# Kernel optimization log

Measured on AMD Instinct MI355X. Metric: run time of the kernel, lower is better.

## Reference

```python
import jax, jax.numpy as jnp
import numpy as np

B, N, DEG = 64, 512, 16        # graphs, nodes per graph, avg degree
C, HID = 10, 128               # input feat dim (== num_classes quirk), hidden
E = B * N * DEG                # total edges (fixed; pooling masks edges)


def _gcn(x, W, b, src, dst, emask, n):
    # PyG GCNConv: add self-loops, symmetric norm D^-1/2 (A+I) D^-1/2 (XW) + b
    h = x @ W
    deg = jax.ops.segment_sum(emask, dst, num_segments=n) + 1.0  # +1 self-loop
    dinv = jax.lax.rsqrt(deg)
    norm = dinv[src] * dinv[dst] * emask
    agg = jax.ops.segment_sum(h[src] * norm[:, None], dst, num_segments=n)
    return agg + h * (dinv * dinv)[:, None] + b  # self-loop term + bias


def _sag_pool(x, src, dst, emask, Wp, bp, n_per):
    # SAGPooling: score = tanh(GCN(x)); per-graph top-k (ratio=0.5); x' = x[perm]*score
    n = x.shape[0]
    score = jnp.tanh(_gcn(x, Wp, bp, src, dst, emask, n)[:, 0])
    k = n_per // 2
    vals, idx = jax.lax.top_k(score.reshape(B, n_per), k)  # [B,k]
    perm = (idx + (jnp.arange(B) * n_per)[:, None]).reshape(-1)
    xk = x[perm] * vals.reshape(-1)[:, None]
    # relabel edges; drop edges touching removed nodes via mask (fixed E)
    mapping = jnp.full((n,), -1, jnp.int32).at[perm].set(
        jnp.arange(B * k, dtype=jnp.int32))
    ns, nd = mapping[src], mapping[dst]
    nmask = emask * ((ns >= 0) & (nd >= 0)).astype(emask.dtype)
    return xk, jnp.maximum(ns, 0), jnp.maximum(nd, 0), nmask, k


def _readout(x, k):
    # global max pool || global mean pool (all kept nodes are real, no padding)
    xg = x.reshape(B, k, -1)
    return jnp.concatenate([xg.max(axis=1), xg.mean(axis=1)], axis=1)


def setup_inputs() -> dict:
    key = jax.random.key(0)
    ks = jax.random.split(key, 16)
    x = jax.random.normal(ks[0], (B * N, C), jnp.float32)
    off = jnp.repeat(jnp.arange(B, dtype=jnp.int32) * N, N * DEG)
    src = jax.random.randint(ks[1], (E,), 0, N, jnp.int32) + off
    dst = jax.random.randint(ks[2], (E,), 0, N, jnp.int32) + off
    p = lambda k, s: jax.random.normal(k, s, jnp.float32) * 0.05
    return {
        "x": x, "src": src, "dst": dst,
        "W1": p(ks[3], (C, HID)), "b1": jnp.zeros((HID,), jnp.float32),
        "W2": p(ks[4], (HID, HID)), "b2": jnp.zeros((HID,), jnp.float32),
        "W3": p(ks[5], (HID, HID)), "b3": jnp.zeros((HID,), jnp.float32),
        "Wp": p(ks[6], (HID, 1)), "bp": jnp.zeros((1,), jnp.float32),
        "L1W": p(ks[7], (2 * HID, HID)), "L1b": jnp.zeros((HID,), jnp.float32),
        "L2W": p(ks[8], (HID, HID // 2)), "L2b": jnp.zeros((HID // 2,), jnp.float32),
    }


def reference(x, src, dst, W1, b1, W2, b2, W3, b3, Wp, bp, L1W, L1b, L2W, L2b):
    emask = jnp.ones((E,), jnp.float32)
    h = jax.nn.relu(_gcn(x, W1, b1, src, dst, emask, B * N))
    h, src, dst, emask, k = _sag_pool(h, src, dst, emask, Wp, bp, N)
    x1 = _readout(h, k)
    h = jax.nn.relu(_gcn(h, W2, b2, src, dst, emask, B * k))
    h, src, dst, emask, k = _sag_pool(h, src, dst, emask, Wp, bp, k)
    x2 = _readout(h, k)
    h = jax.nn.relu(_gcn(h, W3, b3, src, dst, emask, B * k))
    h, src, dst, emask, k = _sag_pool(h, src, dst, emask, Wp, bp, k)
    x3 = _readout(h, k)
    z = x1 + x2 + x3
    z = jax.nn.relu(z @ L1W + L1b)
    # dropout inactive in eval mode
    z = jax.nn.relu(z @ L2W + L2b)
    return jax.nn.log_softmax(z, axis=1)
```

## Files before the change

### kernel.cpp

```cpp
#include <hip/hip_runtime.h>
#include <math.h>

#define BGR 64
#define N0 512
#define E_TOT (BGR*N0*16)
#define EPG 8192
#define EIT 16
#define HID 128


__device__ __forceinline__ int2 ldcoh(const int2* p){
  unsigned long long v = __hip_atomic_load(
      (const unsigned long long*)p, __ATOMIC_RELAXED, __HIP_MEMORY_SCOPE_AGENT);
  int2 r; r.x = (int)(unsigned int)v; r.y = (int)(unsigned int)(v >> 32);
  return r;
}

template<bool COH>
__device__ __forceinline__ int2 lde(const int2* p){
  if (COH) return ldcoh(p);
  return *p;
}

template<bool COH>
__device__ __forceinline__ float score_edges(const int2* __restrict__ csr,
    int start, int c, const float* hloc, int gbase){
  float a = 0.f; int j = 0;
  for (; j + 4 <= c; j += 4){
    int2 e0 = lde<COH>(csr+start+j),   e1 = lde<COH>(csr+start+j+1);
    int2 e2 = lde<COH>(csr+start+j+2), e3 = lde<COH>(csr+start+j+3);
    a += __int_as_float(e0.y)*hloc[e0.x - gbase]
       + __int_as_float(e1.y)*hloc[e1.x - gbase]
       + __int_as_float(e2.y)*hloc[e2.x - gbase]
       + __int_as_float(e3.y)*hloc[e3.x - gbase];
  }
  for (; j < c; j++){
    int2 e = lde<COH>(csr+start+j);
    a += __int_as_float(e.y)*hloc[e.x - gbase];
  }
  return a;
}

__device__ __forceinline__ float4 row_edges_coh(const int2* __restrict__ csr,
    int start, int c, const float4* h4, int gbase, int l){
  float4 acc = make_float4(0.f,0.f,0.f,0.f);
  int j = 0;
  for (; j + 4 <= c; j += 4){
    int2 e0 = ldcoh(csr+start+j),   e1 = ldcoh(csr+start+j+1);
    int2 e2 = ldcoh(csr+start+j+2), e3 = ldcoh(csr+start+j+3);
    float4 h0 = h4[(e0.x - gbase)*32 + l];
    float4 h1 = h4[(e1.x - gbase)*32 + l];
    float4 h2 = h4[(e2.x - gbase)*32 + l];
    float4 h3 = h4[(e3.x - gbase)*32 + l];
    float w0 = __int_as_float(e0.y), w1 = __int_as_float(e1.y);
    float w2 = __int_as_float(e2.y), w3 = __int_as_float(e3.y);
    acc.x += w0*h0.x + w1*h1.x + w2*h2.x + w3*h3.x;
    acc.y += w0*h0.y + w1*h1.y + w2*h2.y + w3*h3.y;
    acc.z += w0*h0.z + w1*h1.z + w2*h2.z + w3*h3.z;
    acc.w += w0*h0.w + w1*h1.w + w2*h2.w + w3*h3.w;
  }
  for (; j < c; j++){
    int2 e = ldcoh(csr+start+j);
    float wgt = __int_as_float(e.y);
    float4 hv = h4[(e.x - gbase)*32 + l];
    acc.x += wgt*hv.x; acc.y += wgt*hv.y; acc.z += wgt*hv.z; acc.w += wgt*hv.w;
  }
  return acc;
}

__device__ __forceinline__ void bitonic_sort(float* sv, int* si, float v, int idx,
                                             int t, int nper, bool act){
  for (int kk = 2; kk <= nper; kk <<= 1){
    for (int jj = kk >> 1; jj > 0; jj >>= 1){
      if (jj >= 64){
        if (act){ sv[t] = v; si[t] = idx; }
        __syncthreads();
        if (act){
          int p = t ^ jj;
          float pv = sv[p]; int pi = si[p];
          bool amLower = (t & jj) == 0;
          bool dirDesc = (t & kk) == 0;
          bool betterMine = (v > pv) || (v == pv && idx < pi);
          if ((amLower == dirDesc) != betterMine){ v = pv; idx = pi; }
        }
        __syncthreads();
      } else if (act){
        float pv = __shfl_xor(v, jj);
        int   pi = __shfl_xor(idx, jj);
        bool amLower = (t & jj) == 0;
        bool dirDesc = (t & kk) == 0;
        bool betterMine = (v > pv) || (v == pv && idx < pi);
        if ((amLower == dirDesc) != betterMine){ v = pv; idx = pi; }
      }
    }
  }
  if (act){ sv[t] = v; si[t] = idx; }
  __syncthreads();
}

template<bool COH>
__device__ __forceinline__ void relabel(int2* __restrict__ edges,
    int2* __restrict__ csr, const int* si, int* map, int* sb, int* cur,
    float* dl, int* rpl, int* cntl, int t, int nper, int k,
    int gbase, int ebase){
  if (t < nper) map[t] = -1;
  if (t < k) sb[t] = 0;
  __syncthreads();
  if (t < k) map[si[t]] = t;
  __syncthreads();
  int2 ebuf[EIT];
  #pragma unroll
  for (int it = 0; it < EIT; it++){
    int i = ebase + it*512 + t;
    int2 e = lde<COH>(edges + i);
    int2 ne = make_int2(-1, 0);
    if (e.x >= 0){
      int ns = map[e.x - gbase], nd = map[e.y - gbase];
      if (ns >= 0 && nd >= 0){
        ne = make_int2(gbase + ns, gbase + nd);
        atomicAdd(&sb[nd], 1);
      }
    }
    ebuf[it] = ne;
    edges[i] = ne;
  }
  __syncthreads();
  int vdeg = (t < k) ? sb[t] : 0;
  for (int off = 1; off < k; off <<= 1){
    int add = (t >= off && t < k) ? sb[t-off] : 0;
    __syncthreads();
    if (t < k) sb[t] += add;
    __syncthreads();
  }
  if (t < k){
    int excl = sb[t] - vdeg;
    rpl[t] = ebase + excl;
    cntl[t] = vdeg;
    cur[t] = excl;
    float dv = rsqrtf((float)vdeg + 1.f);
    dl[t] = dv;
  }
  __syncthreads();
  #pragma unroll
  for (int it = 0; it < EIT; it++){
    int2 e = ebuf[it];
    if (e.x >= 0){
      int sl = e.x - gbase, dc = e.y - gbase;
      int pos = atomicAdd(&cur[dc], 1);
      csr[ebase + pos] = make_int2(e.x, __float_as_int(dl[sl]*dl[dc]));
    }
  }
  __syncthreads();
}

__device__ __forceinline__ void gemm_inplace(float* xl, const float* __restrict__ W,
                                             int nn, int t){
  float4* xl4 = (float4*)xl;
  int fq = t & 31;
  int ng = t >> 5;
  for (int tb = 0; tb < nn; tb += 64){
    int n0 = tb + ng*4;
    float4 acc[4];
    #pragma unroll
    for (int c = 0; c < 4; c++) acc[c] = make_float4(0.f,0.f,0.f,0.f);
    for (int i = 0; i < HID; i += 4){
      float4 w0 = *(const float4*)(W + (i+0)*HID + fq*4);
      float4 w1 = *(const float4*)(W + (i+1)*HID + fq*4);
      float4 w2 = *(const float4*)(W + (i+2)*HID + fq*4);
      float4 w3 = *(const float4*)(W + (i+3)*HID + fq*4);
      #pragma unroll
      for (int c = 0; c < 4; c++){
        float4 xv = *(const float4*)(xl + (n0+c)*HID + i);
        acc[c].x += xv.x*w0.x; acc[c].x += xv.y*w1.x;
        acc[c].x += xv.z*w2.x; acc[c].x += xv.w*w3.x;
        acc[c].y += xv.x*w0.y; acc[c].y += xv.y*w1.y;
        acc[c].y += xv.z*w2.y; acc[c].y += xv.w*w3.y;
        acc[c].z += xv.x*w0.z; acc[c].z += xv.y*w1.z;
        acc[c].z += xv.z*w2.z; acc[c].z += xv.w*w3.z;
        acc[c].w += xv.x*w0.w; acc[c].w += xv.y*w1.w;
        acc[c].w += xv.z*w2.w; acc[c].w += xv.w*w3.w;
      }
    }
    __syncthreads();
    #pragma unroll
    for (int c = 0; c < 4; c++)
      xl4[(n0+c)*32 + fq] = acc[c];
  }
  __syncthreads();
}

__global__ __launch_bounds__(512) void k_topo0(
    const int* __restrict__ s0, const int* __restrict__ d0,
    int2* __restrict__ edges, int* __restrict__ cnt, int* __restrict__ rowptr,
    float* __restrict__ dinv, int2* __restrict__ csr){
  __shared__ int   deg[512];
  __shared__ int   sb[512];
  __shared__ int   cur[512];
  __shared__ float dl[512];
  int g = (blockIdx.x & 7)*8 + (blockIdx.x >> 3);
  int t = threadIdx.x;
  int gbase = g*N0, ebase = g*EPG;
  deg[t] = 0;
  __syncthreads();
  int2 ebuf[EIT];
  #pragma unroll
  for (int it = 0; it < EIT; it++){
    int i = ebase + it*512 + t;
    int2 e = make_int2(s0[i], d0[i]);
    ebuf[it] = e;
    edges[i] = e;
    atomicAdd(&deg[e.y - gbase], 1);
  }
  __syncthreads();
  int vdeg = deg[t];
  sb[t] = vdeg; __syncthreads();
  for (int off = 1; off < 512; off <<= 1){
    int add = (t >= off) ? sb[t-off] : 0;
    __syncthreads(); sb[t] += add; __syncthreads();
  }
  int excl = sb[t] - vdeg;
  rowptr[gbase + t] = ebase + excl;
  cnt[gbase + t] = vdeg;
  cur[t] = excl;
  float dv = rsqrtf((float)vdeg + 1.f);
  dl[t] = dv;
  dinv[gbase + t] = dv;
  __syncthreads();
  #pragma unroll
  for (int it = 0; it < EIT; it++){
    int2 e = ebuf[it];
    int sl = e.x - gbase, dc = e.y - gbase;
    int pos = atomicAdd(&cur[dc], 1);
    csr[ebase + pos] = make_int2(e.x, __float_as_int(dl[sl]*dl[dc]));
  }
}

__global__ __launch_bounds__(512) void k_l1_fused(
    const float* __restrict__ x, const float* __restrict__ W1,
    const int2* __restrict__ csr, const int* __restrict__ rowptr,
    const int* __restrict__ cnt, const float* __restrict__ dinv,
    const float* __restrict__ b1, const float* __restrict__ Wp,
    float4* __restrict__ gout4, float* __restrict__ hp_part){
  extern __shared__ float hl[];
  int b = blockIdx.x;
  int xcd = b & 7, idx = b >> 3;
  int graph = xcd*8 + (idx >> 3);
  int sub = idx & 7;
  int qf = sub >> 1, half = sub & 1;
  int t = threadIdx.x;
  int gbase = graph*N0;
  int fp = t & 31;
  int f = qf*32 + fp;
  float wcol[10];
  #pragma unroll
  for (int k = 0; k < 10; k++) wcol[k] = W1[k*HID + f];
  for (int n = t >> 5; n < N0; n += 16){
    const float* xr = x + (gbase + n)*10;
    float acc = 0.f;
    #pragma unroll
    for (int k = 0; k < 10; k++) acc += xr[k]*wcol[k];
    hl[n*32 + fp] = acc;
  }
  __syncthreads();
  const float4* hl4 = (const float4*)hl;
  int l = t & 7, grp = t >> 3;
  float4 bb = ((const float4*)b1)[qf*8 + l];
  float4 wp = ((const float4*)Wp)[qf*8 + l];
  int n0 = half*256;
  for (int nl = n0 + grp; nl < n0 + 256; nl += 64){
    int node = gbase + nl;
    int start = rowptr[node], c = cnt[node];
    float4 acc = make_float4(0.f,0.f,0.f,0.f);
    int j = 0;
    for (; j + 4 <= c; j += 4){
      int2 e0 = csr[start+j],   e1 = csr[start+j+1];
      int2 e2 = csr[start+j+2], e3 = csr[start+j+3];
      float4 h0 = hl4[(e0.x - gbase)*8 + l];
      float4 h1 = hl4[(e1.x - gbase)*8 + l];
      float4 h2 = hl4[(e2.x - gbase)*8 + l];
      float4 h3 = hl4[(e3.x - gbase)*8 + l];
      float w0 = __int_as_float(e0.y), w1 = __int_as_float(e1.y);
      float w2 = __int_as_float(e2.y), w3 = __int_as_float(e3.y);
      acc.x += w0*h0.x + w1*h1.x + w2*h2.x + w3*h3.x;
      acc.y += w0*h0.y + w1*h1.y + w2*h2.y + w3*h3.y;
      acc.z += w0*h0.z + w1*h1.z + w2*h2.z + w3*h3.z;
      acc.w += w0*h0.w + w1*h1.w + w2*h2.w + w3*h3.w;
    }
    for (; j < c; j++){
      int2 e = csr[start + j];
      float wgt = __int_as_float(e.y);
      float4 hv = hl4[(e.x - gbase)*8 + l];
      acc.x += wgt*hv.x; acc.y += wgt*hv.y; acc.z += wgt*hv.z; acc.w += wgt*hv.w;
    }
    float di = dinv[node], dd = di*di;
    float4 hs = hl4[nl*8 + l];
    float4 v;
    v.x = fmaxf(acc.x + hs.x*dd + bb.x, 0.f);
    v.y = fmaxf(acc.y + hs.y*dd + bb.y, 0.f);
    v.z = fmaxf(acc.z + hs.z*dd + bb.z, 0.f);
    v.w = fmaxf(acc.w + hs.w*dd + bb.w, 0.f);
    gout4[node*32 + qf*8 + l] = v;
    float contrib = v.x*wp.x + v.y*wp.y + v.z*wp.z + v.w*wp.w;
    #pragma unroll
    for (int off = 4; off; off >>= 1) contrib += __shfl_down(contrib, off, 8);
    if (l == 0) hp_part[qf*32768 + node] = contrib;
  }
}

__global__ __launch_bounds__(512) void k_tail(
    const float4* __restrict__ gout4, const float* __restrict__ hp_part,
    int2* __restrict__ csr, int2* __restrict__ edges,
    const int* __restrict__ rowptr1, const int* __restrict__ cnt1,
    const float* __restrict__ dinv1, const float* __restrict__ bp,
    const float* __restrict__ W2, const float* __restrict__ b2,
    const float* __restrict__ W3, const float* __restrict__ b3,
    const float* __restrict__ Wp,
    const float* __restrict__ L1W, const float* __restrict__ L1b,
    const float* __restrict__ L2W, const float* __restrict__ L2b,
    float* __restrict__ out){
  __shared__ float xl[256*HID];
  __shared__ float sv[512];
  __shared__ int   si[512];
  __shared__ float hpl[512];
  __shared__ union UU {
    struct { int map[512]; int sb[512]; int cur[256]; } r;
    float4 pr[2][16][32];
  } u;
  __shared__ float dl[256];
  __shared__ int   rpl[256];
  __shared__ int   cntl[256];
  __shared__ float zacc[256];
  __shared__ float red[2];

  int g = (blockIdx.x & 7)*8 + (blockIdx.x >> 3);
  int t = threadIdx.x;
  int gbase = g*N0, ebase = g*EPG;
  int l = t & 31, j0 = t >> 5;
  float4* xl4 = (float4*)xl;
  float bp0 = bp[0];

  {
    int node = gbase + t;
    hpl[t] = hp_part[node] + hp_part[32768 + node]
           + hp_part[65536 + node] + hp_part[98304 + node];
  }
  __syncthreads();
  {
    int start = rowptr1[gbase + t], c = cnt1[gbase + t];
    float a = score_edges<false>(csr, start, c, hpl, gbase);
    float di = dinv1[gbase + t];
    float v = tanhf(a + hpl[t]*di*di + bp0);
    bitonic_sort(sv, si, v, t, t, 512, true);
  }
  {
    float4 mx = make_float4(-INFINITY,-INFINITY,-INFINITY,-INFINITY);
    float4 sm = make_float4(0.f,0.f,0.f,0.f);
    for (int j = j0; j < 256; j += 16){
      float val = sv[j]; int row = si[j];
      float4 hv = gout4[(gbase + row)*32 + l];
      float4 o = make_float4(hv.x*val, hv.y*val, hv.z*val, hv.w*val);
      xl4[j*32 + l] = o;
      mx.x = fmaxf(mx.x, o.x); mx.y = fmaxf(mx.y, o.y);
      mx.z = fmaxf(mx.z, o.z); mx.w = fmaxf(mx.w, o.w);
      sm.x += o.x; sm.y += o.y; sm.z += o.z; sm.w += o.w;
    }
    u.pr[0][j0][l] = mx; u.pr[1][j0][l] = sm;
    __syncthreads();
    if (t < 32){
      float4 M = u.pr[0][0][t], S = u.pr[1][0][t];
      #pragma unroll
      for (int q = 1; q < 16; q++){
        float4 m2 = u.pr[0][q][t], s2 = u.pr[1][q][t];
        M.x = fmaxf(M.x, m2.x); M.y = fmaxf(M.y, m2.y);
        M.z = fmaxf(M.z, m2.z); M.w = fmaxf(M.w, m2.w);
        S.x += s2.x; S.y += s2.y; S.z += s2.z; S.w += s2.w;
      }
      float ki = 1.f/256.f;
      zacc[t*4+0] = M.x; zacc[t*4+1] = M.y; zacc[t*4+2] = M.z; zacc[t*4+3] = M.w;
      zacc[128+t*4+0] = S.x*ki; zacc[128+t*4+1] = S.y*ki;
      zacc[128+t*4+2] = S.z*ki; zacc[128+t*4+3] = S.w*ki;
    }
    __syncthreads();
  }
  relabel<false>(edges, csr, si, u.r.map, u.r.sb, u.r.cur, dl, rpl, cntl,
                 t, 512, 256, gbase, ebase);

  gemm_inplace(xl, W2, 256, t);
  {
    float4 bb = ((const float4*)b2)[l];
    float4 wp = ((const float4*)Wp)[l];
    for (int r = 0; r < 16; r++){
      int n = r*16 + j0;
      float4 acc = row_edges_coh(csr, rpl[n], cntl[n], xl4, gbase, l);
      float di = dl[n], dd = di*di;
      float4 hs = xl4[n*32 + l];
      float4 v;
      v.x = fmaxf(acc.x + hs.x*dd + bb.x, 0.f);
      v.y = fmaxf(acc.y + hs.y*dd + bb.y, 0.f);
      v.z = fmaxf(acc.z + hs.z*dd + bb.z, 0.f);
      v.w = fmaxf(acc.w + hs.w*dd + bb.w, 0.f);
      float contrib = v.x*wp.x + v.y*wp.y + v.z*wp.z + v.w*wp.w;
      #pragma unroll
      for (int off = 16; off; off >>= 1) contrib += __shfl_down(contrib, off, 32);
      if (l == 0) hpl[n] = contrib;
    }
  }
  __syncthreads();

  {
    float v = 0.f;
    if (t < 256){
      float a = score_edges<true>(csr, rpl[t], cntl[t], hpl, gbase);
      float di = dl[t];
      v = tanhf(a + hpl[t]*di*di + bp0);
    }
    bitonic_sort(sv, si, v, t, t, 256, t < 256);
  }
  {
    float4 bb = ((const float4*)b2)[l];
    float4 o[8];
    float4 mx = make_float4(-INFINITY,-INFINITY,-INFINITY,-INFINITY);
    float4 sm = make_float4(0.f,0.f,0.f,0.f);
    #pragma unroll
    for (int r = 0; r < 8; r++){
      int j = j0 + 16*r;
      float val = sv[j]; int row = si[j];
      float4 acc = row_edges_coh(csr, rpl[row], cntl[row], xl4, gbase, l);
      float di = dl[row], dd = di*di;
      float4 hs = xl4[row*32 + l];
      float4 v;
      v.x = fmaxf(acc.x + hs.x*dd + bb.x, 0.f);
      v.y = fmaxf(acc.y + hs.y*dd + bb.y, 0.f);
      v.z = fmaxf(acc.z + hs.z*dd + bb.z, 0.f);
      v.w = fmaxf(acc.w + hs.w*dd + bb.w, 0.f);
      float4 ov = make_float4(v.x*val, v.y*val, v.z*val, v.w*val);
      o[r] = ov;
      mx.x = fmaxf(mx.x, ov.x); mx.y = fmaxf(mx.y, ov.y);
      mx.z = fmaxf(mx.z, ov.z); mx.w = fmaxf(mx.w, ov.w);
      sm.x += ov.x; sm.y += ov.y; sm.z += ov.z; sm.w += ov.w;
    }
    u.pr[0][j0][l] = mx; u.pr[1][j0][l] = sm;
    __syncthreads();
    #pragma unroll
    for (int r = 0; r < 8; r++){ int j = j0 + 16*r; xl4[j*32 + l] = o[r]; }
    if (t < 32){
      float4 M = u.pr[0][0][t], S = u.pr[1][0][t];
      #pragma unroll
      for (int q = 1; q < 16; q++){
        float4 m2 = u.pr[0][q][t], s2 = u.pr[1][q][t];
        M.x = fmaxf(M.x, m2.x); M.y = fmaxf(M.y, m2.y);
        M.z = fmaxf(M.z, m2.z); M.w = fmaxf(M.w, m2.w);
        S.x += s2.x; S.y += s2.y; S.z += s2.z; S.w += s2.w;
      }
      float ki = 1.f/128.f;
      zacc[t*4+0] += M.x; zacc[t*4+1] += M.y; zacc[t*4+2] += M.z; zacc[t*4+3] += M.w;
      zacc[128+t*4+0] += S.x*ki; zacc[128+t*4+1] += S.y*ki;
      zacc[128+t*4+2] += S.z*ki; zacc[128+t*4+3] += S.w*ki;
    }
    __syncthreads();
  }
  relabel<true>(edges, csr, si, u.r.map, u.r.sb, u.r.cur, dl, rpl, cntl,
                t, 256, 128, gbase, ebase);

  gemm_inplace(xl, W3, 128, t);
  {
    float4 bb = ((const float4*)b3)[l];
    float4 wp = ((const float4*)Wp)[l];
    for (int r = 0; r < 8; r++){
      int n = r*16 + j0;
      float4 acc = row_edges_coh(csr, rpl[n], cntl[n], xl4, gbase, l);
      float di = dl[n], dd = di*di;
      float4 hs = xl4[n*32 + l];
      float4 v;
      v.x = fmaxf(acc.x + hs.x*dd + bb.x, 0.f);
      v.y = fmaxf(acc.y + hs.y*dd + bb.y, 0.f);
      v.z = fmaxf(acc.z + hs.z*dd + bb.z, 0.f);
      v.w = fmaxf(acc.w + hs.w*dd + bb.w, 0.f);
      float contrib = v.x*wp.x + v.y*wp.y + v.z*wp.z + v.w*wp.w;
      #pragma unroll
      for (int off = 16; off; off >>= 1) contrib += __shfl_down(contrib, off, 32);
      if (l == 0) hpl[n] = contrib;
    }
  }
  __syncthreads();

  {
    float v = 0.f;
    if (t < 128){
      float a = score_edges<true>(csr, rpl[t], cntl[t], hpl, gbase);
      float di = dl[t];
      v = tanhf(a + hpl[t]*di*di + bp0);
    }
    bitonic_sort(sv, si, v, t, t, 128, t < 128);
  }
  {
    float4 bb = ((const float4*)b3)[l];
    float4 mx = make_float4(-INFINITY,-INFINITY,-INFINITY,-INFINITY);
    float4 sm = make_float4(0.f,0.f,0.f,0.f);
    #pragma unroll
    for (int r = 0; r < 4; r++){
      int j = j0 + 16*r;
      float val = sv[j]; int row = si[j];
      float4 acc = row_edges_coh(csr, rpl[row], cntl[row], xl4, gbase, l);
      float di = dl[row], dd = di*di;
      float4 hs = xl4[row*32 + l];
      float4 v;
      v.x = fmaxf(acc.x + hs.x*dd + bb.x, 0.f);
      v.y = fmaxf(acc.y + hs.y*dd + bb.y, 0.f);
      v.z = fmaxf(acc.z + hs.z*dd + bb.z, 0.f);
      v.w = fmaxf(acc.w + hs.w*dd + bb.w, 0.f);
      float4 ov = make_float4(v.x*val, v.y*val, v.z*val, v.w*val);
      mx.x = fmaxf(mx.x, ov.x); mx.y = fmaxf(mx.y, ov.y);
      mx.z = fmaxf(mx.z, ov.z); mx.w = fmaxf(mx.w, ov.w);
      sm.x += ov.x; sm.y += ov.y; sm.z += ov.z; sm.w += ov.w;
    }
    u.pr[0][j0][l] = mx; u.pr[1][j0][l] = sm;
    __syncthreads();
    if (t < 32){
      float4 M = u.pr[0][0][t], S = u.pr[1][0][t];
      #pragma unroll
      for (int q = 1; q < 16; q++){
        float4 m2 = u.pr[0][q][t], s2 = u.pr[1][q][t];
        M.x = fmaxf(M.x, m2.x); M.y = fmaxf(M.y, m2.y);
        M.z = fmaxf(M.z, m2.z); M.w = fmaxf(M.w, m2.w);
        S.x += s2.x; S.y += s2.y; S.z += s2.z; S.w += s2.w;
      }
      float ki = 1.f/64.f;
      zacc[t*4+0] += M.x; zacc[t*4+1] += M.y; zacc[t*4+2] += M.z; zacc[t*4+3] += M.w;
      zacc[128+t*4+0] += S.x*ki; zacc[128+t*4+1] += S.y*ki;
      zacc[128+t*4+2] += S.z*ki; zacc[128+t*4+3] += S.w*ki;
    }
    __syncthreads();
  }
  if (t < 128){
    float a = L1b[t];
    for (int i = 0; i < 256; i++) a += zacc[i]*L1W[i*128 + t];
    sv[t] = fmaxf(a, 0.f);
  }
  __syncthreads();
  if (t < 64){
    float a = L2b[t];
    for (int i = 0; i < 128; i++) a += sv[i]*L2W[i*64 + t];
    hpl[t] = fmaxf(a, 0.f);
  }
  __syncthreads();
  if (t == 0){
    float mxv = -INFINITY;
    for (int i = 0; i < 64; i++) mxv = fmaxf(mxv, hpl[i]);
    float s = 0.f;
    for (int i = 0; i < 64; i++) s += expf(hpl[i] - mxv);
    red[0] = mxv; red[1] = logf(s);
  }
  __syncthreads();
  if (t < 64) out[g*64 + t] = hpl[t] - red[0] - red[1];
}

extern "C" void kernel_launch(void* const* d_in, const int* in_sizes, int n_in,
                              void* d_out, int out_size, void* d_ws, size_t ws_size,
                              hipStream_t stream){
  (void)in_sizes; (void)n_in; (void)out_size; (void)ws_size;
  const float* x0  = (const float*)d_in[0];
  const int*   s0  = (const int*)  d_in[1];
  const int*   d0  = (const int*)  d_in[2];
  const float* W1  = (const float*)d_in[3];  const float* b1 = (const float*)d_in[4];
  const float* W2  = (const float*)d_in[5];  const float* b2 = (const float*)d_in[6];
  const float* W3  = (const float*)d_in[7];  const float* b3 = (const float*)d_in[8];
  const float* Wp  = (const float*)d_in[9];  const float* bp = (const float*)d_in[10];
  const float* L1W = (const float*)d_in[11]; const float* L1b = (const float*)d_in[12];
  const float* L2W = (const float*)d_in[13]; const float* L2b = (const float*)d_in[14];
  float* out = (float*)d_out;

  float* w = (float*)d_ws;
  float* gout  = w; w += 32768*HID;
  float* dinvv = w; w += 32768;
  float* hppt  = w; w += 4*32768;
  int* cnt     = (int*)w; w += 32768;
  int* rowptr  = (int*)w; w += 32768;
  int2* edges  = (int2*)w; w += 2*E_TOT;
  int2* csr    = (int2*)w; w += 2*E_TOT;

  k_topo0<<<BGR, 512, 0, stream>>>(s0, d0, edges, cnt, rowptr, dinvv, csr);
  k_l1_fused<<<512, 512, 65536, stream>>>(x0, W1, csr, rowptr, cnt, dinvv,
                                          b1, Wp, (float4*)gout, hppt);
  k_tail<<<BGR, 512, 0, stream>>>((const float4*)gout, hppt, csr, edges,
                                  rowptr, cnt, dinvv, bp, W2, b2, W3, b3, Wp,
                                  L1W, L1b, L2W, L2b, out);
}
```

Before: 268.0 us.

## Split tail kernel across four blocks per graph with feature-slice partitioning

The tail kernel previously ran one block per graph (64 blocks). It now launches four blocks per graph, each owning a 32-wide feature slice, and uses spin-wait global barriers on per-graph atomic counters to exchange partial pooling scores and activations through global memory. Each block redundantly recomputes the top-k selection and edge relabeling on its own copy of the edge and CSR buffers. Shared memory per block shrinks and uses an XOR-swizzled layout to avoid bank conflicts. This adds global traffic, a redundant topology pass per block, and a risk of deadlock if the four blocks of a graph are not co-resident.

```diff
diff --git a/kernel.cpp b/kernel.cpp
--- a/kernel.cpp
+++ b/kernel.cpp
@@ -7,6 +7,8 @@
 #define EPG 8192
 #define EIT 16
 #define HID 128
+
+#define XLI(row,l4) (((row)<<3) | (((l4) ^ (row)) & 7))
 
 
 __device__ __forceinline__ int2 ldcoh(const int2* p){
@@ -41,17 +43,18 @@
   return a;
 }
 
-__device__ __forceinline__ float4 row_edges_coh(const int2* __restrict__ csr,
-    int start, int c, const float4* h4, int gbase, int l){
+__device__ __forceinline__ float4 gcn_row(const int2* __restrict__ csr,
+    int start, int c, const float4* xl4, int gbase, int l, int row,
+    float dd, float4 bb){
   float4 acc = make_float4(0.f,0.f,0.f,0.f);
   int j = 0;
   for (; j + 4 <= c; j += 4){
-    int2 e0 = ldcoh(csr+start+j),   e1 = ldcoh(csr+start+j+1);
-    int2 e2 = ldcoh(csr+start+j+2), e3 = ldcoh(csr+start+j+3);
-    float4 h0 = h4[(e0.x - gbase)*32 + l];
-    float4 h1 = h4[(e1.x - gbase)*32 + l];
-    float4 h2 = h4[(e2.x - gbase)*32 + l];
-    float4 h3 = h4[(e3.x - gbase)*32 + l];
+    int2 e0 = csr[start+j],   e1 = csr[start+j+1];
+    int2 e2 = csr[start+j+2], e3 = csr[start+j+3];
+    float4 h0 = xl4[XLI(e0.x - gbase, l)];
+    float4 h1 = xl4[XLI(e1.x - gbase, l)];
+    float4 h2 = xl4[XLI(e2.x - gbase, l)];
+    float4 h3 = xl4[XLI(e3.x - gbase, l)];
     float w0 = __int_as_float(e0.y), w1 = __int_as_float(e1.y);
     float w2 = __int_as_float(e2.y), w3 = __int_as_float(e3.y);
     acc.x += w0*h0.x + w1*h1.x + w2*h2.x + w3*h3.x;
@@ -60,12 +63,18 @@
     acc.w += w0*h0.w + w1*h1.w + w2*h2.w + w3*h3.w;
   }
   for (; j < c; j++){
-    int2 e = ldcoh(csr+start+j);
+    int2 e = csr[start + j];
     float wgt = __int_as_float(e.y);
-    float4 hv = h4[(e.x - gbase)*32 + l];
+    float4 hv = xl4[XLI(e.x - gbase, l)];
     acc.x += wgt*hv.x; acc.y += wgt*hv.y; acc.z += wgt*hv.z; acc.w += wgt*hv.w;
   }
-  return acc;
+  float4 hs = xl4[XLI(row, l)];
+  float4 v;
+  v.x = fmaxf(acc.x + hs.x*dd + bb.x, 0.f);
+  v.y = fmaxf(acc.y + hs.y*dd + bb.y, 0.f);
+  v.z = fmaxf(acc.z + hs.z*dd + bb.z, 0.f);
+  v.w = fmaxf(acc.w + hs.w*dd + bb.w, 0.f);
+  return v;
 }
 
 __device__ __forceinline__ void bitonic_sort(float* sv, int* si, float v, int idx,
@@ -98,31 +107,30 @@
   __syncthreads();
 }
 
-template<bool COH>
-__device__ __forceinline__ void relabel(int2* __restrict__ edges,
-    int2* __restrict__ csr, const int* si, int* map, int* sb, int* cur,
-    float* dl, int* rpl, int* cntl, int t, int nper, int k,
-    int gbase, int ebase){
-  if (t < nper) map[t] = -1;
+__device__ __forceinline__ void relabel4(const int2* __restrict__ esrc, int sbase,
+    int2* __restrict__ edst, int dbase, int2* __restrict__ csr, int cbase,
+    const int* si, int* map_, int* sb, int* cur, float* dl, int* rpl, int* cntl,
+    int t, int nper, int k, int gbase){
+  if (t < nper) map_[t] = -1;
   if (t < k) sb[t] = 0;
   __syncthreads();
-  if (t < k) map[si[t]] = t;
+  if (t < k) map_[si[t]] = t;
   __syncthreads();
   int2 ebuf[EIT];
   #pragma unroll
   for (int it = 0; it < EIT; it++){
-    int i = ebase + it*512 + t;
-    int2 e = lde<COH>(edges + i);
+    int slot = it*512 + t;
+    int2 e = esrc[sbase + slot];
     int2 ne = make_int2(-1, 0);
     if (e.x >= 0){
-      int ns = map[e.x - gbase], nd = map[e.y - gbase];
+      int ns = map_[e.x - gbase], nd = map_[e.y - gbase];
       if (ns >= 0 && nd >= 0){
         ne = make_int2(gbase + ns, gbase + nd);
         atomicAdd(&sb[nd], 1);
       }
     }
     ebuf[it] = ne;
-    edges[i] = ne;
+    edst[dbase + slot] = ne;
   }
   __syncthreads();
   int vdeg = (t < k) ? sb[t] : 0;
@@ -134,7 +142,7 @@
   }
   if (t < k){
     int excl = sb[t] - vdeg;
-    rpl[t] = ebase + excl;
+    rpl[t] = cbase + excl;
     cntl[t] = vdeg;
     cur[t] = excl;
     float dv = rsqrtf((float)vdeg + 1.f);
@@ -147,52 +155,81 @@
     if (e.x >= 0){
       int sl = e.x - gbase, dc = e.y - gbase;
       int pos = atomicAdd(&cur[dc], 1);
-      csr[ebase + pos] = make_int2(e.x, __float_as_int(dl[sl]*dl[dc]));
-    }
-  }
-  __syncthreads();
-}
-
-__device__ __forceinline__ void gemm_inplace(float* xl, const float* __restrict__ W,
-                                             int nn, int t){
-  float4* xl4 = (float4*)xl;
-  int fq = t & 31;
-  int ng = t >> 5;
-  for (int tb = 0; tb < nn; tb += 64){
-    int n0 = tb + ng*4;
-    float4 acc[4];
-    #pragma unroll
-    for (int c = 0; c < 4; c++) acc[c] = make_float4(0.f,0.f,0.f,0.f);
-    for (int i = 0; i < HID; i += 4){
-      float4 w0 = *(const float4*)(W + (i+0)*HID + fq*4);
-      float4 w1 = *(const float4*)(W + (i+1)*HID + fq*4);
-      float4 w2 = *(const float4*)(W + (i+2)*HID + fq*4);
-      float4 w3 = *(const float4*)(W + (i+3)*HID + fq*4);
-      #pragma unroll
-      for (int c = 0; c < 4; c++){
-        float4 xv = *(const float4*)(xl + (n0+c)*HID + i);
-        acc[c].x += xv.x*w0.x; acc[c].x += xv.y*w1.x;
-        acc[c].x += xv.z*w2.x; acc[c].x += xv.w*w3.x;
-        acc[c].y += xv.x*w0.y; acc[c].y += xv.y*w1.y;
-        acc[c].y += xv.z*w2.y; acc[c].y += xv.w*w3.y;
-        acc[c].z += xv.x*w0.z; acc[c].z += xv.y*w1.z;
-        acc[c].z += xv.z*w2.z; acc[c].z += xv.w*w3.z;
-        acc[c].w += xv.x*w0.w; acc[c].w += xv.y*w1.w;
-        acc[c].w += xv.z*w2.w; acc[c].w += xv.w*w3.w;
-      }
-    }
-    __syncthreads();
-    #pragma unroll
-    for (int c = 0; c < 4; c++)
-      xl4[(n0+c)*32 + fq] = acc[c];
-  }
-  __syncthreads();
+      csr[cbase + pos] = make_int2(e.x, __float_as_int(dl[sl]*dl[dc]));
+    }
+  }
+  __syncthreads();
+}
+
+template<int NT>
+__device__ __forceinline__ void gemm_slice(const float* __restrict__ xg,
+    const float* __restrict__ W, float4* xl4, int t, int s){
+  int f4 = t & 7, ng = t >> 3;
+  const float* Wb = W + s*32 + f4*4;
+  float4 acc[NT];
+  #pragma unroll
+  for (int c = 0; c < NT; c++) acc[c] = make_float4(0.f,0.f,0.f,0.f);
+  for (int i = 0; i < HID; i += 4){
+    float4 w0 = *(const float4*)(Wb + (i+0)*HID);
+    float4 w1 = *(const float4*)(Wb + (i+1)*HID);
+    float4 w2 = *(const float4*)(Wb + (i+2)*HID);
+    float4 w3 = *(const float4*)(Wb + (i+3)*HID);
+    #pragma unroll
+    for (int c = 0; c < NT; c++){
+      float4 xv = *(const float4*)(xg + (ng + 64*c)*HID + i);
+      acc[c].x += xv.x*w0.x; acc[c].x += xv.y*w1.x;
+      acc[c].x += xv.z*w2.x; acc[c].x += xv.w*w3.x;
+      acc[c].y += xv.x*w0.y; acc[c].y += xv.y*w1.y;
+      acc[c].y += xv.z*w2.y; acc[c].y += xv.w*w3.y;
+      acc[c].z += xv.x*w0.z; acc[c].z += xv.y*w1.z;
+      acc[c].z += xv.z*w2.z; acc[c].z += xv.w*w3.z;
+      acc[c].w += xv.x*w0.w; acc[c].w += xv.y*w1.w;
+      acc[c].w += xv.z*w2.w; acc[c].w += xv.w*w3.w;
+    }
+  }
+  #pragma unroll
+  for (int c = 0; c < NT; c++) xl4[XLI(ng + 64*c, f4)] = acc[c];
+}
+
+__device__ __forceinline__ void zacc_pass(const float* xl, float zp[][8][32],
+    float* zsl, int R, int init, int t){
+  if (t < 256){
+    int q = t >> 5, f = t & 31;
+    float m = -INFINITY, sm = 0.f;
+    for (int r = q; r < R; r += 8){
+      float vv = xl[XLI(r, f >> 2)*4 + (f & 3)];
+      m = fmaxf(m, vv); sm += vv;
+    }
+    zp[0][q][f] = m; zp[1][q][f] = sm;
+  }
+  __syncthreads();
+  if (t < 32){
+    float m = zp[0][0][t], sm = zp[1][0][t];
+    #pragma unroll
+    for (int q = 1; q < 8; q++){ m = fmaxf(m, zp[0][q][t]); sm += zp[1][q][t]; }
+    float ki = 1.f/(float)R;
+    if (init){ zsl[t] = m; zsl[32+t] = sm*ki; }
+    else     { zsl[t] += m; zsl[32+t] += sm*ki; }
+  }
+  __syncthreads();
+}
+
+__device__ __forceinline__ void gsync(int* c, int t){
+  __threadfence();
+  __syncthreads();
+  if (t == 0){
+    __hip_atomic_fetch_add(c, 1, __ATOMIC_ACQ_REL, __HIP_MEMORY_SCOPE_AGENT);
+    while (__hip_atomic_load(c, __ATOMIC_ACQUIRE, __HIP_MEMORY_SCOPE_AGENT) < 4)
+      __builtin_amdgcn_s_sleep(4);
+  }
+  __syncthreads();
+  __threadfence();
 }
 
 __global__ __launch_bounds__(512) void k_topo0(
     const int* __restrict__ s0, const int* __restrict__ d0,
     int2* __restrict__ edges, int* __restrict__ cnt, int* __restrict__ rowptr,
-    float* __restrict__ dinv, int2* __restrict__ csr){
+    float* __restrict__ dinv, int2* __restrict__ csr, int* __restrict__ syncc){
   __shared__ int   deg[512];
   __shared__ int   sb[512];
   __shared__ int   cur[512];
@@ -200,6 +237,7 @@
   int g = (blockIdx.x & 7)*8 + (blockIdx.x >> 3);
   int t = threadIdx.x;
   int gbase = g*N0, ebase = g*EPG;
+  if (t < 8) syncc[g*8 + t] = 0;
   deg[t] = 0;
   __syncthreads();
   int2 ebuf[EIT];
@@ -307,252 +345,212 @@
   }
 }
 
-__global__ __launch_bounds__(512) void k_tail(
-    const float4* __restrict__ gout4, const float* __restrict__ hp_part,
-    int2* __restrict__ csr, int2* __restrict__ edges,
+__global__ __launch_bounds__(512) void k_tail4(
+    const float4* __restrict__ gout4, const float* __restrict__ hppt,
+    const int2* __restrict__ edges1, const int2* __restrict__ csr1,
     const int* __restrict__ rowptr1, const int* __restrict__ cnt1,
-    const float* __restrict__ dinv1, const float* __restrict__ bp,
+    const float* __restrict__ dinv1,
+    int2* __restrict__ edges4, int2* __restrict__ csr4,
+    float* __restrict__ x2g, float* __restrict__ x3g,
+    float* __restrict__ hp2, float* __restrict__ hp3,
+    float* __restrict__ zg, int* __restrict__ syncc,
+    const float* __restrict__ bp,
     const float* __restrict__ W2, const float* __restrict__ b2,
     const float* __restrict__ W3, const float* __restrict__ b3,
     const float* __restrict__ Wp,
     const float* __restrict__ L1W, const float* __restrict__ L1b,
     const float* __restrict__ L2W, const float* __restrict__ L2b,
     float* __restrict__ out){
-  __shared__ float xl[256*HID];
+  __shared__ float xl[256*32];
   __shared__ float sv[512];
   __shared__ int   si[512];
   __shared__ float hpl[512];
-  __shared__ union UU {
-    struct { int map[512]; int sb[512]; int cur[256]; } r;
-    float4 pr[2][16][32];
-  } u;
+  __shared__ int   map_[512];
+  __shared__ int   sb[512];
+  __shared__ int   cur[256];
   __shared__ float dl[256];
   __shared__ int   rpl[256];
   __shared__ int   cntl[256];
-  __shared__ float zacc[256];
+  __shared__ float zp[2][8][32];
+  __shared__ float zsl[64];
   __shared__ float red[2];
 
-  int g = (blockIdx.x & 7)*8 + (blockIdx.x >> 3);
+  int b = blockIdx.x;
+  int jb = b & 63, s = b >> 6;
+  int g = (jb & 7)*8 + (jb >> 3);
   int t = threadIdx.x;
-  int gbase = g*N0, ebase = g*EPG;
-  int l = t & 31, j0 = t >> 5;
+  int gbase = g*N0;
+  int ebase  = (s*BGR + g)*EPG;
+  int ebase0 = g*EPG;
+  int l = t & 7, grp = t >> 3;
   float4* xl4 = (float4*)xl;
   float bp0 = bp[0];
+  int* sc = syncc + g*8;
 
   {
     int node = gbase + t;
-    hpl[t] = hp_part[node] + hp_part[32768 + node]
-           + hp_part[65536 + node] + hp_part[98304 + node];
+    hpl[t] = hppt[node] + hppt[32768+node] + hppt[65536+node] + hppt[98304+node];
   }
   __syncthreads();
   {
     int start = rowptr1[gbase + t], c = cnt1[gbase + t];
-    float a = score_edges<false>(csr, start, c, hpl, gbase);
+    float a = score_edges<false>(csr1, start, c, hpl, gbase);
     float di = dinv1[gbase + t];
     float v = tanhf(a + hpl[t]*di*di + bp0);
     bitonic_sort(sv, si, v, t, t, 512, true);
   }
-  {
-    float4 mx = make_float4(-INFINITY,-INFINITY,-INFINITY,-INFINITY);
-    float4 sm = make_float4(0.f,0.f,0.f,0.f);
-    for (int j = j0; j < 256; j += 16){
-      float val = sv[j]; int row = si[j];
-      float4 hv = gout4[(gbase + row)*32 + l];
-      float4 o = make_float4(hv.x*val, hv.y*val, hv.z*val, hv.w*val);
-      xl4[j*32 + l] = o;
-      mx.x = fmaxf(mx.x, o.x); mx.y = fmaxf(mx.y, o.y);
-      mx.z = fmaxf(mx.z, o.z); mx.w = fmaxf(mx.w, o.w);
-      sm.x += o.x; sm.y += o.y; sm.z += o.z; sm.w += o.w;
-    }
-    u.pr[0][j0][l] = mx; u.pr[1][j0][l] = sm;
-    __syncthreads();
-    if (t < 32){
-      float4 M = u.pr[0][0][t], S = u.pr[1][0][t];
-      #pragma unroll
-      for (int q = 1; q < 16; q++){
-        float4 m2 = u.pr[0][q][t], s2 = u.pr[1][q][t];
-        M.x = fmaxf(M.x, m2.x); M.y = fmaxf(M.y, m2.y);
-        M.z = fmaxf(M.z, m2.z); M.w = fmaxf(M.w, m2.w);
-        S.x += s2.x; S.y += s2.y; S.z += s2.z; S.w += s2.w;
-      }
-      float ki = 1.f/256.f;
-      zacc[t*4+0] = M.x; zacc[t*4+1] = M.y; zacc[t*4+2] = M.z; zacc[t*4+3] = M.w;
-      zacc[128+t*4+0] = S.x*ki; zacc[128+t*4+1] = S.y*ki;
-      zacc[128+t*4+2] = S.z*ki; zacc[128+t*4+3] = S.w*ki;
-    }
-    __syncthreads();
-  }
-  relabel<false>(edges, csr, si, u.r.map, u.r.sb, u.r.cur, dl, rpl, cntl,
-                 t, 512, 256, gbase, ebase);
-
-  gemm_inplace(xl, W2, 256, t);
-  {
-    float4 bb = ((const float4*)b2)[l];
-    float4 wp = ((const float4*)Wp)[l];
-    for (int r = 0; r < 16; r++){
-      int n = r*16 + j0;
-      float4 acc = row_edges_coh(csr, rpl[n], cntl[n], xl4, gbase, l);
-      float di = dl[n], dd = di*di;
-      float4 hs = xl4[n*32 + l];
-      float4 v;
-      v.x = fmaxf(acc.x + hs.x*dd + bb.x, 0.f);
-      v.y = fmaxf(acc.y + hs.y*dd + bb.y, 0.f);
-      v.z = fmaxf(acc.z + hs.z*dd + bb.z, 0.f);
-      v.w = fmaxf(acc.w + hs.w*dd + bb.w, 0.f);
+  #pragma unroll
+  for (int p = 0; p < 4; p++){
+    int jr = grp + 64*p;
+    float val = sv[jr]; int row = si[jr];
+    float4 hv = gout4[(gbase + row)*32 + s*8 + l];
+    float4 o = make_float4(hv.x*val, hv.y*val, hv.z*val, hv.w*val);
+    xl4[XLI(jr, l)] = o;
+    *(float4*)(x2g + (g*256 + jr)*HID + s*32 + l*4) = o;
+  }
+  __syncthreads();
+  zacc_pass(xl, zp, zsl, 256, 1, t);
+  relabel4(edges1, g*EPG, edges4, ebase, csr4, ebase,
+           si, map_, sb, cur, dl, rpl, cntl, t, 512, 256, gbase);
+  gsync(sc + 0, t);
+
+  gemm_slice<4>(x2g + g*256*HID, W2, xl4, t, s);
+  __syncthreads();
+  {
+    float4 bb = ((const float4*)b2)[s*8 + l];
+    float4 wp = ((const float4*)Wp)[s*8 + l];
+    #pragma unroll
+    for (int p = 0; p < 4; p++){
+      int row = grp + 64*p;
+      float dd = dl[row]*dl[row];
+      float4 v = gcn_row(csr4, rpl[row], cntl[row], xl4, gbase, l, row, dd, bb);
       float contrib = v.x*wp.x + v.y*wp.y + v.z*wp.z + v.w*wp.w;
       #pragma unroll
-      for (int off = 16; off; off >>= 1) contrib += __shfl_down(contrib, off, 32);
-      if (l == 0) hpl[n] = contrib;
-    }
-  }
-  __syncthreads();
-
+      for (int off = 4; off; off >>= 1) contrib += __shfl_down(contrib, off, 8);
+      if (l == 0) hp2[s*32768 + gbase + row] = contrib;
+    }
+  }
+  gsync(sc + 1, t);
+
+  if (t < 256){
+    int node = gbase + t;
+    hpl[t] = hp2[node] + hp2[32768+node] + hp2[65536+node] + hp2[98304+node];
+  }
+  __syncthreads();
   {
     float v = 0.f;
     if (t < 256){
-      float a = score_edges<true>(csr, rpl[t], cntl[t], hpl, gbase);
-      float di = dl[t];
-      v = tanhf(a + hpl[t]*di*di + bp0);
+      int st0 = rpl[t] - ebase + ebase0;
+      float a = score_edges<true>(csr4, st0, cntl[t], hpl, gbase);
+      v = tanhf(a + hpl[t]*dl[t]*dl[t] + bp0);
     }
     bitonic_sort(sv, si, v, t, t, 256, t < 256);
   }
   {
-    float4 bb = ((const float4*)b2)[l];
-    float4 o[8];
-    float4 mx = make_float4(-INFINITY,-INFINITY,-INFINITY,-INFINITY);
-    float4 sm = make_float4(0.f,0.f,0.f,0.f);
-    #pragma unroll
-    for (int r = 0; r < 8; r++){
-      int j = j0 + 16*r;
-      float val = sv[j]; int row = si[j];
-      float4 acc = row_edges_coh(csr, rpl[row], cntl[row], xl4, gbase, l);
-      float di = dl[row], dd = di*di;
-      float4 hs = xl4[row*32 + l];
-      float4 v;
-      v.x = fmaxf(acc.x + hs.x*dd + bb.x, 0.f);
-      v.y = fmaxf(acc.y + hs.y*dd + bb.y, 0.f);
-      v.z = fmaxf(acc.z + hs.z*dd + bb.z, 0.f);
-      v.w = fmaxf(acc.w + hs.w*dd + bb.w, 0.f);
-      float4 ov = make_float4(v.x*val, v.y*val, v.z*val, v.w*val);
-      o[r] = ov;
-      mx.x = fmaxf(mx.x, ov.x); mx.y = fmaxf(mx.y, ov.y);
-      mx.z = fmaxf(mx.z, ov.z); mx.w = fmaxf(mx.w, ov.w);
-      sm.x += ov.x; sm.y += ov.y; sm.z += ov.z; sm.w += ov.w;
-    }
-    u.pr[0][j0][l] = mx; u.pr[1][j0][l] = sm;
+    float4 bb = ((const float4*)b2)[s*8 + l];
+    float4 ov[2];
+    #pragma unroll
+    for (int p = 0; p < 2; p++){
+      int jr = grp + 64*p;
+      float val = sv[jr]; int row = si[jr];
+      float dd = dl[row]*dl[row];
+      float4 v = gcn_row(csr4, rpl[row], cntl[row], xl4, gbase, l, row, dd, bb);
+      ov[p] = make_float4(v.x*val, v.y*val, v.z*val, v.w*val);
+      *(float4*)(x3g + (g*128 + jr)*HID + s*32 + l*4) = ov[p];
+    }
     __syncthreads();
     #pragma unroll
-    for (int r = 0; r < 8; r++){ int j = j0 + 16*r; xl4[j*32 + l] = o[r]; }
-    if (t < 32){
-      float4 M = u.pr[0][0][t], S = u.pr[1][0][t];
-      #pragma unroll
-      for (int q = 1; q < 16; q++){
-        float4 m2 = u.pr[0][q][t], s2 = u.pr[1][q][t];
-        M.x = fmaxf(M.x, m2.x); M.y = fmaxf(M.y, m2.y);
-        M.z = fmaxf(M.z, m2.z); M.w = fmaxf(M.w, m2.w);
-        S.x += s2.x; S.y += s2.y; S.z += s2.z; S.w += s2.w;
-      }
-      float ki = 1.f/128.f;
-      zacc[t*4+0] += M.x; zacc[t*4+1] += M.y; zacc[t*4+2] += M.z; zacc[t*4+3] += M.w;
-      zacc[128+t*4+0] += S.x*ki; zacc[128+t*4+1] += S.y*ki;
-      zacc[128+t*4+2] += S.z*ki; zacc[128+t*4+3] += S.w*ki;
-    }
-    __syncthreads();
-  }
-  relabel<true>(edges, csr, si, u.r.map, u.r.sb, u.r.cur, dl, rpl, cntl,
-                t, 256, 128, gbase, ebase);
-
-  gemm_inplace(xl, W3, 128, t);
-  {
-    float4 bb = ((const float4*)b3)[l];
-    float4 wp = ((const float4*)Wp)[l];
-    for (int r = 0; r < 8; r++){
-      int n = r*16 + j0;
-      float4 acc = row_edges_coh(csr, rpl[n], cntl[n], xl4, gbase, l);
-      float di = dl[n], dd = di*di;
-      float4 hs = xl4[n*32 + l];
-      float4 v;
-      v.x = fmaxf(acc.x + hs.x*dd + bb.x, 0.f);
-      v.y = fmaxf(acc.y + hs.y*dd + bb.y, 0.f);
-      v.z = fmaxf(acc.z + hs.z*dd + bb.z, 0.f);
-      v.w = fmaxf(acc.w + hs.w*dd + bb.w, 0.f);
+    for (int p = 0; p < 2; p++) xl4[XLI(grp + 64*p, l)] = ov[p];
+  }
+  __syncthreads();
+  zacc_pass(xl, zp, zsl, 128, 0, t);
+  relabel4(edges4, ebase, edges4, ebase, csr4, ebase,
+           si, map_, sb, cur, dl, rpl, cntl, t, 256, 128, gbase);
+  gsync(sc + 2, t);
+
+  gemm_slice<2>(x3g + g*128*HID, W3, xl4, t, s);
+  __syncthreads();
+  {
+    float4 bb = ((const float4*)b3)[s*8 + l];
+    float4 wp = ((const float4*)Wp)[s*8 + l];
+    #pragma unroll
+    for (int p = 0; p < 2; p++){
+      int row = grp + 64*p;
+      float dd = dl[row]*dl[row];
+      float4 v = gcn_row(csr4, rpl[row], cntl[row], xl4, gbase, l, row, dd, bb);
       float contrib = v.x*wp.x + v.y*wp.y + v.z*wp.z + v.w*wp.w;
       #pragma unroll
-      for (int off = 16; off; off >>= 1) contrib += __shfl_down(contrib, off, 32);
-      if (l == 0) hpl[n] = contrib;
-    }
-  }
-  __syncthreads();
-
+      for (int off = 4; off; off >>= 1) contrib += __shfl_down(contrib, off, 8);
+      if (l == 0) hp3[s*32768 + gbase + row] = contrib;
+    }
+  }
+  gsync(sc + 3, t);
+
+  if (t < 128){
+    int node = gbase + t;
+    hpl[t] = hp3[node] + hp3[32768+node] + hp3[65536+node] + hp3[98304+node];
+  }
+  __syncthreads();
   {
     float v = 0.f;
     if (t < 128){
-      float a = score_edges<true>(csr, rpl[t], cntl[t], hpl, gbase);
-      float di = dl[t];
-      v = tanhf(a + hpl[t]*di*di + bp0);
+      int st0 = rpl[t] - ebase + ebase0;
+      float a = score_edges<true>(csr4, st0, cntl[t], hpl, gbase);
+      v = tanhf(a + hpl[t]*dl[t]*dl[t] + bp0);
     }
     bitonic_sort(sv, si, v, t, t, 128, t < 128);
   }
   {
-    float4 bb = ((const float4*)b3)[l];
-    float4 mx = make_float4(-INFINITY,-INFINITY,-INFINITY,-INFINITY);
-    float4 sm = make_float4(0.f,0.f,0.f,0.f);
-    #pragma unroll
-    for (int r = 0; r < 4; r++){
-      int j = j0 + 16*r;
-      float val = sv[j]; int row = si[j];
-      float4 acc = row_edges_coh(csr, rpl[row], cntl[row], xl4, gbase, l);
-      float di = dl[row], dd = di*di;
-      float4 hs = xl4[row*32 + l];
-      float4 v;
-      v.x = fmaxf(acc.x + hs.x*dd + bb.x, 0.f);
-      v.y = fmaxf(acc.y + hs.y*dd + bb.y, 0.f);
-      v.z = fmaxf(acc.z + hs.z*dd + bb.z, 0.f);
-      v.w = fmaxf(acc.w + hs.w*dd + bb.w, 0.f);
-      float4 ov = make_float4(v.x*val, v.y*val, v.z*val, v.w*val);
-      mx.x = fmaxf(mx.x, ov.x); mx.y = fmaxf(mx.y, ov.y);
-      mx.z = fmaxf(mx.z, ov.z); mx.w = fmaxf(mx.w, ov.w);
-      sm.x += ov.x; sm.y += ov.y; sm.z += ov.z; sm.w += ov.w;
-    }
-    u.pr[0][j0][l] = mx; u.pr[1][j0][l] = sm;
+    float4 bb = ((const float4*)b3)[s*8 + l];
+    int jr = grp;
+    float val = sv[jr]; int row = si[jr];
+    float dd = dl[row]*dl[row];
+    float4 v = gcn_row(csr4, rpl[row], cntl[row], xl4, gbase, l, row, dd, bb);
+    float4 ov = make_float4(v.x*val, v.y*val, v.z*val, v.w*val);
     __syncthreads();
-    if (t < 32){
-      float4 M = u.pr[0][0][t], S = u.pr[1][0][t];
-      #pragma unroll
-      for (int q = 1; q < 16; q++){
-        float4 m2 = u.pr[0][q][t], s2 = u.pr[1][q][t];
-        M.x = fmaxf(M.x, m2.x); M.y = fmaxf(M.y, m2.y);
-        M.z = fmaxf(M.z, m2.z); M.w = fmaxf(M.w, m2.w);
-        S.x += s2.x; S.y += s2.y; S.z += s2.z; S.w += s2.w;
-      }
-      float ki = 1.f/64.f;
-      zacc[t*4+0] += M.x; zacc[t*4+1] += M.y; zacc[t*4+2] += M.z; zacc[t*4+3] += M.w;
-      zacc[128+t*4+0] += S.x*ki; zacc[128+t*4+1] += S.y*ki;
-      zacc[128+t*4+2] += S.z*ki; zacc[128+t*4+3] += S.w*ki;
-    }
-    __syncthreads();
-  }
+    xl4[XLI(jr, l)] = ov;
+  }
+  __syncthreads();
+  zacc_pass(xl, zp, zsl, 64, 0, t);
+  if (t < 64){
+    int pos = (t < 32) ? (s*32 + t) : (96 + s*32 + t);
+    zg[g*256 + pos] = zsl[t];
+  }
+  __threadfence();
+  __syncthreads();
+  if (t == 0)
+    __hip_atomic_fetch_add(sc + 4, 1, __ATOMIC_ACQ_REL, __HIP_MEMORY_SCOPE_AGENT);
+  if (s != 0) return;
+  if (t == 0){
+    while (__hip_atomic_load(sc + 4, __ATOMIC_ACQUIRE, __HIP_MEMORY_SCOPE_AGENT) < 4)
+      __builtin_amdgcn_s_sleep(4);
+  }
+  __syncthreads();
+  __threadfence();
+
+  if (t < 256) hpl[t] = zg[g*256 + t];
+  __syncthreads();
   if (t < 128){
     float a = L1b[t];
-    for (int i = 0; i < 256; i++) a += zacc[i]*L1W[i*128 + t];
+    for (int i = 0; i < 256; i++) a += hpl[i]*L1W[i*128 + t];
     sv[t] = fmaxf(a, 0.f);
   }
   __syncthreads();
   if (t < 64){
     float a = L2b[t];
     for (int i = 0; i < 128; i++) a += sv[i]*L2W[i*64 + t];
-    hpl[t] = fmaxf(a, 0.f);
+    hpl[256 + t] = fmaxf(a, 0.f);
   }
   __syncthreads();
   if (t == 0){
     float mxv = -INFINITY;
-    for (int i = 0; i < 64; i++) mxv = fmaxf(mxv, hpl[i]);
-    float s = 0.f;
-    for (int i = 0; i < 64; i++) s += expf(hpl[i] - mxv);
-    red[0] = mxv; red[1] = logf(s);
-  }
-  __syncthreads();
-  if (t < 64) out[g*64 + t] = hpl[t] - red[0] - red[1];
+    for (int i = 0; i < 64; i++) mxv = fmaxf(mxv, hpl[256+i]);
+    float sx = 0.f;
+    for (int i = 0; i < 64; i++) sx += expf(hpl[256+i] - mxv);
+    red[0] = mxv; red[1] = logf(sx);
+  }
+  __syncthreads();
+  if (t < 64) out[g*64 + t] = hpl[256+t] - red[0] - red[1];
 }
 
 extern "C" void kernel_launch(void* const* d_in, const int* in_sizes, int n_in,
@@ -574,15 +572,26 @@
   float* gout  = w; w += 32768*HID;
   float* dinvv = w; w += 32768;
   float* hppt  = w; w += 4*32768;
-  int* cnt     = (int*)w; w += 32768;
-  int* rowptr  = (int*)w; w += 32768;
-  int2* edges  = (int2*)w; w += 2*E_TOT;
-  int2* csr    = (int2*)w; w += 2*E_TOT;
-
-  k_topo0<<<BGR, 512, 0, stream>>>(s0, d0, edges, cnt, rowptr, dinvv, csr);
-  k_l1_fused<<<512, 512, 65536, stream>>>(x0, W1, csr, rowptr, cnt, dinvv,
+  float* x2g   = w; w += BGR*256*HID;
+  float* x3g   = w; w += BGR*128*HID;
+  float* hp2   = w; w += 4*32768;
+  float* hp3   = w; w += 4*32768;
+  float* zg    = w; w += BGR*256;
+  int*  cnt1    = (int*)w; w += 32768;
+  int*  rowptr1 = (int*)w; w += 32768;
+  int*  syncc   = (int*)w; w += 1024;
+  int2* edges1 = (int2*)w; w += 2*E_TOT;
+  int2* csr1   = (int2*)w; w += 2*E_TOT;
+  int2* edges4 = (int2*)w; w += 8*E_TOT;
+  int2* csr4   = (int2*)w; w += 8*E_TOT;
+
+  k_topo0<<<BGR, 512, 0, stream>>>(s0, d0, edges1, cnt1, rowptr1, dinvv, csr1,
+                                   syncc);
+  k_l1_fused<<<512, 512, 65536, stream>>>(x0, W1, csr1, rowptr1, cnt1, dinvv,
                                           b1, Wp, (float4*)gout, hppt);
-  k_tail<<<BGR, 512, 0, stream>>>((const float4*)gout, hppt, csr, edges,
-                                  rowptr, cnt, dinvv, bp, W2, b2, W3, b3, Wp,
-                                  L1W, L1b, L2W, L2b, out);
-}
+  k_tail4<<<4*BGR, 512, 0, stream>>>((const float4*)gout, hppt,
+                                     edges1, csr1, rowptr1, cnt1, dinvv,
+                                     edges4, csr4, x2g, x3g, hp2, hp3, zg,
+                                     syncc, bp, W2, b2, W3, b3, Wp,
+                                     L1W, L1b, L2W, L2b, out);
+}
```

Measured after the change: 576.3 us. 115% more time.
